# Kernel optimization log

Hardware: AMD Instinct MI355X
Metric: run time of the kernel (lower is better)

The kernel has to match this reference:

```python
import jax, jax.numpy as jnp
import numpy as np

B, T, DIM, H, KV, HD = 1, 2048, 2048, 16, 4, 128


def _rope_tables(T, hd):
    half = hd // 2
    inv_freq = 1.0 / (10000.0 ** (np.arange(0, half, dtype=np.float32) / half))
    t = np.arange(T, dtype=np.float32)
    freqs = np.outer(t, inv_freq)                # [T, hd/2]
    emb = np.concatenate([freqs, freqs], axis=-1)  # [T, hd]
    return jnp.asarray(np.cos(emb)), jnp.asarray(np.sin(emb))


def setup_inputs() -> dict:
    key = jax.random.key(0)
    kx, kq, kk, kv, ko = jax.random.split(key, 5)
    s = 0.02
    x = jax.random.normal(kx, (B, T, DIM), dtype=jnp.float32)
    wq = jax.random.normal(kq, (H * HD, DIM), dtype=jnp.float32) * s
    wk = jax.random.normal(kk, (KV * HD, DIM), dtype=jnp.float32) * s
    wv = jax.random.normal(kv, (KV * HD, DIM), dtype=jnp.float32) * s
    wo = jax.random.normal(ko, (DIM, H * HD), dtype=jnp.float32) * s
    cos, sin = _rope_tables(T, HD)
    return {"x": x, "wq": wq, "wk": wk, "wv": wv, "wo": wo, "cos": cos, "sin": sin}


def _rotate_half(u):
    u1, u2 = jnp.split(u, 2, axis=-1)
    return jnp.concatenate([-u2, u1], axis=-1)


def _apply_rope(u, cos, sin):
    # u: [B, T, h, hd]; cos/sin: [T, hd]
    c = cos[None, :, None, :]
    s = sin[None, :, None, :]
    return u * c + _rotate_half(u) * s


def reference(x, wq, wk, wv, wo, cos, sin):
    b, t, dim = x.shape
    hd = cos.shape[1]
    h = wq.shape[0] // hd
    kvh = wk.shape[0] // hd
    rep = h // kvh
    scale = hd ** -0.5

    q = (x @ wq.T).reshape(b, t, h, hd)
    k = (x @ wk.T).reshape(b, t, kvh, hd)
    v = (x @ wv.T).reshape(b, t, kvh, hd)

    q = _apply_rope(q, cos, sin)
    k = _apply_rope(k, cos, sin)

    # Group queries by shared KV head instead of materializing repeat_kv
    qg = q.reshape(b, t, kvh, rep, hd)
    scores = jnp.einsum('bqgrd,bkgd->bgrqk', qg, k) * scale  # [b,g,r,T,T]
    causal = jnp.tril(jnp.ones((t, t), dtype=bool))
    scores = jnp.where(causal[None, None, None], scores, jnp.float32(-1e30))
    attn = jax.nn.softmax(scores, axis=-1)
    out = jnp.einsum('bgrqk,bkgd->bqgrd', attn, v).reshape(b, t, h * hd)
    return out @ wo.T
```

## Files before the change

### kernel.cpp

```cpp
#include <hip/hip_runtime.h>
#include <hip/hip_bf16.h>

typedef unsigned short u16;
typedef __attribute__((ext_vector_type(8))) short bf16x8;
typedef __attribute__((ext_vector_type(8))) unsigned short u16x8;
typedef __attribute__((ext_vector_type(4))) float f32x4;

#define T_SEQ 2048
#define DIM   2048
#define NH    16
#define NKV   4
#define HD    128
#define NQKV  3072
#define SCALE 0.08838834764831845f
#define CHUNK 512

__device__ __forceinline__ u16 f2bf(float f) {
  unsigned int u = __float_as_uint(f);
  unsigned int r = (u + 0x7fffu + ((u >> 16) & 1u)) >> 16;
  return (u16)r;
}
__device__ __forceinline__ float bf2f(u16 v) {
  return __uint_as_float(((unsigned int)v) << 16);
}

#define B1 1048576
#define B2 2097152
#define B3 2359296
#define B4 2621440
#define B5 3670016
__global__ void cast_all(const float4* __restrict__ x,  const float4* __restrict__ wq,
                         const float4* __restrict__ wk, const float4* __restrict__ wv,
                         const float4* __restrict__ wo,
                         ushort4* __restrict__ xb, ushort4* __restrict__ wqkvb,
                         ushort4* __restrict__ wob) {
  int i = blockIdx.x * 256 + threadIdx.x;
  const float4* src; ushort4* dst; int j;
  if (i < B1)      { src = x;  dst = xb;               j = i; }
  else if (i < B2) { src = wq; dst = wqkvb;            j = i - B1; }
  else if (i < B3) { src = wk; dst = wqkvb + 1048576;  j = i - B2; }
  else if (i < B4) { src = wv; dst = wqkvb + 1310720;  j = i - B3; }
  else             { src = wo; dst = wob;              j = i - B4; }
  float4 v = src[j];
  ushort4 o;
  o.x = f2bf(v.x); o.y = f2bf(v.y); o.z = f2bf(v.z); o.w = f2bf(v.w);
  dst[j] = o;
}

#define BM 128
#define BN 64
#define BK 64
#define LDP 72

__global__ __launch_bounds__(256) void gemm_bt(
    const u16* __restrict__ A, const u16* __restrict__ W,
    float* __restrict__ Cf, u16* __restrict__ Cb, int M, int N, int K)
{
  __shared__ u16 As[BM * LDP];
  __shared__ u16 Bs[BN * LDP];
  const int tid  = threadIdx.x;
  const int lane = tid & 63;
  const int wave = tid >> 6;
  const int ln   = lane & 15;
  const int quad = lane >> 4;
  const int m0 = blockIdx.y * BM;
  const int n0 = blockIdx.x * BN;
  const int wm = wave * 32;

  const int sr = tid >> 3;
  const int sc = (tid & 7) * 8;

  f32x4 acc[2][4] = {};

  for (int k0 = 0; k0 < K; k0 += BK) {
#pragma unroll
    for (int c = 0; c < 4; ++c) {
      int row = c * 32 + sr;
      *(bf16x8*)&As[row * LDP + sc] =
          *(const bf16x8*)&A[(size_t)(m0 + row) * K + k0 + sc];
    }
#pragma unroll
    for (int c = 0; c < 2; ++c) {
      int row = c * 32 + sr;
      *(bf16x8*)&Bs[row * LDP + sc] =
          *(const bf16x8*)&W[(size_t)(n0 + row) * K + k0 + sc];
    }
    __syncthreads();
#pragma unroll
    for (int ks = 0; ks < 2; ++ks) {
      bf16x8 af[2], bfr[4];
#pragma unroll
      for (int mt = 0; mt < 2; ++mt)
        af[mt] = *(const bf16x8*)&As[(wm + mt * 16 + ln) * LDP + ks * 32 + quad * 8];
#pragma unroll
      for (int nt = 0; nt < 4; ++nt)
        bfr[nt] = *(const bf16x8*)&Bs[(nt * 16 + ln) * LDP + ks * 32 + quad * 8];
#pragma unroll
      for (int mt = 0; mt < 2; ++mt)
#pragma unroll
        for (int nt = 0; nt < 4; ++nt)
          acc[mt][nt] = __builtin_amdgcn_mfma_f32_16x16x32_bf16(
              af[mt], bfr[nt], acc[mt][nt], 0, 0, 0);
    }
    __syncthreads();
  }

#pragma unroll
  for (int mt = 0; mt < 2; ++mt)
#pragma unroll
    for (int nt = 0; nt < 4; ++nt)
#pragma unroll
      for (int r = 0; r < 4; ++r) {
        int row = m0 + wm + mt * 16 + quad * 4 + r;
        int col = n0 + nt * 16 + ln;
        if (Cb) Cb[(size_t)row * N + col] = f2bf(acc[mt][nt][r]);
        else    Cf[(size_t)row * N + col] = acc[mt][nt][r];
      }
}

__global__ __launch_bounds__(256) void rope_fused(
    const u16* __restrict__ QKVb, const float* __restrict__ cosT,
    const float* __restrict__ sinT, u16* __restrict__ Qs,
    u16* __restrict__ Kb, u16* __restrict__ Vt)
{
  const int blk = blockIdx.x, tid = threadIdx.x;
  if (blk < 2048) {
    int e = blk * 2048 + tid * 8;
    int t = e >> 11, rem = e & 2047;
    int h = rem >> 7, d0 = rem & 127;
    const u16* row = QKVb + (size_t)t * NQKV + h * HD;
    u16x8 v = *(const u16x8*)&row[d0];
    u16x8 p = *(const u16x8*)&row[d0 ^ 64];
    float4 c0 = *(const float4*)&cosT[t * HD + d0];
    float4 c1 = *(const float4*)&cosT[t * HD + d0 + 4];
    float4 s0 = *(const float4*)&sinT[t * HD + d0];
    float4 s1 = *(const float4*)&sinT[t * HD + d0 + 4];
    float cc[8] = {c0.x, c0.y, c0.z, c0.w, c1.x, c1.y, c1.z, c1.w};
    float ss[8] = {s0.x, s0.y, s0.z, s0.w, s1.x, s1.y, s1.z, s1.w};
    float sgn = (d0 < 64) ? -1.f : 1.f;
    u16x8 o;
#pragma unroll
    for (int j = 0; j < 8; ++j)
      o[j] = f2bf((bf2f(v[j]) * cc[j] + sgn * bf2f(p[j]) * ss[j]) * SCALE);
    *(u16x8*)&Qs[(size_t)(t * NH + h) * HD + d0] = o;
  } else if (blk < 2560) {
    int e = (blk - 2048) * 2048 + tid * 8;
    int t = e >> 9, rem = e & 511;
    int g = rem >> 7, d0 = rem & 127;
    const u16* row = QKVb + (size_t)t * NQKV + DIM + g * HD;
    u16x8 v = *(const u16x8*)&row[d0];
    u16x8 p = *(const u16x8*)&row[d0 ^ 64];
    float4 c0 = *(const float4*)&cosT[t * HD + d0];
    float4 c1 = *(const float4*)&cosT[t * HD + d0 + 4];
    float4 s0 = *(const float4*)&sinT[t * HD + d0];
    float4 s1 = *(const float4*)&sinT[t * HD + d0 + 4];
    float cc[8] = {c0.x, c0.y, c0.z, c0.w, c1.x, c1.y, c1.z, c1.w};
    float ss[8] = {s0.x, s0.y, s0.z, s0.w, s1.x, s1.y, s1.z, s1.w};
    float sgn = (d0 < 64) ? -1.f : 1.f;
    u16x8 o;
#pragma unroll
    for (int j = 0; j < 8; ++j)
      o[j] = f2bf(bf2f(v[j]) * cc[j] + sgn * bf2f(p[j]) * ss[j]);
    *(u16x8*)&Kb[((size_t)g * T_SEQ + t) * HD + d0] = o;
  } else {
    __shared__ u16 Vls[64][72];
    int bv = blk - 2560;
    int g  = bv >> 6, rem = bv & 63;
    int dt = rem >> 5, tt = rem & 31;
    int t0 = tt * 64, db = dt * 64;
    {
      int lr = tid >> 2, lc = (tid & 3) * 16;
      const u16* src = QKVb + (size_t)(t0 + lr) * NQKV + DIM + NKV * HD + g * HD + db + lc;
      *(u16x8*)&Vls[lr][lc]     = *(const u16x8*)&src[0];
      *(u16x8*)&Vls[lr][lc + 8] = *(const u16x8*)&src[8];
    }
    __syncthreads();
    {
      int dr = tid >> 2, tc = (tid & 3) * 16;
      u16x8 a, b;
#pragma unroll
      for (int j = 0; j < 8; ++j) {
        a[j] = Vls[tc + j][dr];
        b[j] = Vls[tc + 8 + j][dr];
      }
      u16* dst = Vt + (size_t)(g * HD + db + dr) * T_SEQ + t0 + tc;
      *(u16x8*)&dst[0] = a;
      *(u16x8*)&dst[8] = b;
    }
  }
}

#define KSP 136
#define VSP 72
#define PSP 72
__global__ __launch_bounds__(256) void flash_partial(
    const u16* __restrict__ Qs, const u16* __restrict__ Kb,
    const u16* __restrict__ Vt, u16* __restrict__ Opart,
    float* __restrict__ lpart)
{
  const int c  = blockIdx.x;
  const int qi = blockIdx.y;
  const int h  = blockIdx.z;
  const int b  = qi >> 2;
  if (c > b) return;
  const int g  = h >> 2;
  const int q0 = qi << 7;
  const int k0 = c << 9;
  const int kend = min(k0 + CHUNK, q0 + 128);

  __shared__ u16 Ks[64 * KSP];
  __shared__ u16 Vs[HD * VSP];
  __shared__ u16 Ps[4][32 * PSP];

  const int tid  = threadIdx.x;
  const int lane = tid & 63;
  const int w    = tid >> 6;
  const int ln   = lane & 15;
  const int quad = lane >> 4;

  bf16x8 aq[2][4];
#pragma unroll
  for (int mt = 0; mt < 2; ++mt) {
    const u16* qp = Qs + ((size_t)(q0 + w * 32 + mt * 16 + ln) * NH + h) * HD + quad * 8;
#pragma unroll
    for (int ks = 0; ks < 4; ++ks) aq[mt][ks] = *(const bf16x8*)&qp[ks * 32];
  }

  f32x4 o[2][8] = {};
  float rs[2][4] = {};

  const int rb0 = q0 + w * 32 + quad * 4;
  const int rb1 = rb0 + 16;
  const int rmax0 = q0 + w * 32 + 15;
  const int rmax1 = q0 + w * 32 + 31;

  const u16* kbase = Kb + (size_t)g * T_SEQ * HD;

  for (int jb = k0; jb < kend; jb += 64) {
    {
      int r = tid >> 4, cc = (tid & 15) * 8;
#pragma unroll
      for (int i = 0; i < 4; ++i) {
        int row = i * 16 + r;
        *(bf16x8*)&Ks[row * KSP + cc] =
            *(const bf16x8*)&kbase[(size_t)(jb + row) * HD + cc];
      }
    }
    {
      int r = tid >> 3, cc = (tid & 7) * 8;
#pragma unroll
      for (int i = 0; i < 4; ++i) {
        int row = i * 32 + r;
        *(bf16x8*)&Vs[row * VSP + cc] =
            *(const bf16x8*)&Vt[(size_t)(g * HD + row) * T_SEQ + jb + cc];
      }
    }
    __syncthreads();

    if (jb <= rmax1) {
      const bool do0  = (jb <= rmax0);
      const bool diag = (jb >= q0);

#pragma unroll
      for (int nb = 0; nb < 4; ++nb) {
        bf16x8 kf[4];
#pragma unroll
        for (int ks = 0; ks < 4; ++ks)
          kf[ks] = *(const bf16x8*)&Ks[(nb * 16 + ln) * KSP + ks * 32 + quad * 8];
        f32x4 s0 = {}, s1 = {};
#pragma unroll
        for (int ks = 0; ks < 4; ++ks) {
          if (do0) s0 = __builtin_amdgcn_mfma_f32_16x16x32_bf16(aq[0][ks], kf[ks], s0, 0, 0, 0);
          s1 = __builtin_amdgcn_mfma_f32_16x16x32_bf16(aq[1][ks], kf[ks], s1, 0, 0, 0);
        }
        const int j = jb + nb * 16 + ln;
#pragma unroll
        for (int r = 0; r < 4; ++r) {
          if (do0) {
            float p = (!diag || j <= rb0 + r) ? __expf(s0[r]) : 0.f;
            rs[0][r] += p;
            Ps[w][(quad * 4 + r) * PSP + nb * 16 + ln] = f2bf(p);
          }
          float p1 = (!diag || j <= rb1 + r) ? __expf(s1[r]) : 0.f;
          rs[1][r] += p1;
          Ps[w][(16 + quad * 4 + r) * PSP + nb * 16 + ln] = f2bf(p1);
        }
      }

#pragma unroll
      for (int kst = 0; kst < 2; ++kst) {
        bf16x8 ap0, ap1;
        if (do0) ap0 = *(const bf16x8*)&Ps[w][ln * PSP + kst * 32 + quad * 8];
        ap1 = *(const bf16x8*)&Ps[w][(16 + ln) * PSP + kst * 32 + quad * 8];
#pragma unroll
        for (int nb8 = 0; nb8 < 8; ++nb8) {
          bf16x8 bv = *(const bf16x8*)&Vs[(nb8 * 16 + ln) * VSP + kst * 32 + quad * 8];
          if (do0) o[0][nb8] = __builtin_amdgcn_mfma_f32_16x16x32_bf16(ap0, bv, o[0][nb8], 0, 0, 0);
          o[1][nb8] = __builtin_amdgcn_mfma_f32_16x16x32_bf16(ap1, bv, o[1][nb8], 0, 0, 0);
        }
      }
    }
    __syncthreads();
  }

  const int slot = h * 40 + 2 * b * (b + 1) + (qi & 3) * (b + 1) + c;
  u16*   op = Opart + (size_t)slot * (128 * 128);
  float* lp = lpart + (size_t)slot * 128;
#pragma unroll
  for (int mt = 0; mt < 2; ++mt) {
#pragma unroll
    for (int r = 0; r < 4; ++r)
#pragma unroll
      for (int off = 1; off < 16; off <<= 1)
        rs[mt][r] += __shfl_xor(rs[mt][r], off);
    int rowb = w * 32 + mt * 16 + quad * 4;
#pragma unroll
    for (int r = 0; r < 4; ++r) {
#pragma unroll
      for (int nb8 = 0; nb8 < 8; ++nb8)
        op[(rowb + r) * 128 + nb8 * 16 + ln] = f2bf(o[mt][nb8][r]);
      if (ln == 0) lp[rowb + r] = rs[mt][r];
    }
  }
}

__global__ __launch_bounds__(256) void flash_reduce(
    const u16* __restrict__ Opart, const float* __restrict__ lpart,
    u16* __restrict__ AO)
{
  const int h = blockIdx.y;
  const int tid = threadIdx.x;
  const int dgrp = tid & 15, trow = tid >> 4;
  const int t = blockIdx.x * 16 + trow;
  const int d0 = dgrp * 8;
  const int qi = t >> 7, r = t & 127;
  const int b = qi >> 2;
  const int base = h * 40 + 2 * b * (b + 1) + (qi & 3) * (b + 1);
  float so[8] = {};
  float sl = 0.f;
  for (int cc = 0; cc <= b; ++cc) {
    u16x8 ov = *(const u16x8*)&Opart[(size_t)(base + cc) * (128 * 128) + r * 128 + d0];
#pragma unroll
    for (int j = 0; j < 8; ++j) so[j] += bf2f(ov[j]);
    sl += lpart[(size_t)(base + cc) * 128 + r];
  }
  const float inv = 1.f / sl;
  u16x8 o;
#pragma unroll
  for (int j = 0; j < 8; ++j) o[j] = f2bf(so[j] * inv);
  *(u16x8*)&AO[(size_t)t * DIM + h * HD + d0] = o;
}

extern "C" void kernel_launch(void* const* d_in, const int* in_sizes, int n_in,
                              void* d_out, int out_size, void* d_ws, size_t ws_size,
                              hipStream_t stream) {
  const float* x    = (const float*)d_in[0];
  const float* wq   = (const float*)d_in[1];
  const float* wk   = (const float*)d_in[2];
  const float* wv   = (const float*)d_in[3];
  const float* wo   = (const float*)d_in[4];
  const float* cosT = (const float*)d_in[5];
  const float* sinT = (const float*)d_in[6];
  float* out = (float*)d_out;

  char* ws = (char*)d_ws;
  const size_t MB = 1024 * 1024;
  u16*   xb    = (u16*)(ws + 0 * MB);
  u16*   wqkvb = (u16*)(ws + 8 * MB);
  u16*   wob   = (u16*)(ws + 20 * MB);
  u16*   QKVb  = (u16*)(ws + 28 * MB);
  u16*   Qs    = (u16*)(ws + 8 * MB);
  u16*   Kb    = (u16*)(ws + 16 * MB);
  u16*   Vt    = (u16*)(ws + 18 * MB);
  u16*   AO    = (u16*)(ws + 0 * MB);
  u16*   Opart = (u16*)(ws + 28 * MB);
  float* lpart = (float*)(ws + 48 * MB);

  cast_all<<<B5 / 256, 256, 0, stream>>>(
      (const float4*)x, (const float4*)wq, (const float4*)wk, (const float4*)wv,
      (const float4*)wo, (ushort4*)xb, (ushort4*)wqkvb, (ushort4*)wob);

  gemm_bt<<<dim3(NQKV / BN, T_SEQ / BM), 256, 0, stream>>>(
      xb, wqkvb, nullptr, QKVb, T_SEQ, NQKV, DIM);

  rope_fused<<<2816, 256, 0, stream>>>(QKVb, cosT, sinT, Qs, Kb, Vt);

  flash_partial<<<dim3(4, 16, 16), 256, 0, stream>>>(Qs, Kb, Vt, Opart, lpart);
  flash_reduce<<<dim3(T_SEQ / 16, NH), 256, 0, stream>>>(Opart, lpart, AO);

  gemm_bt<<<dim3(DIM / BN, T_SEQ / BM), 256, 0, stream>>>(
      AO, wob, out, nullptr, T_SEQ, DIM, DIM);
}
```

Baseline: 257.6 us.

## Split-K the QKV projection GEMM and fold the partial sum into RoPE

The QKV GEMM is now split into two K halves on a third grid dimension, doubling the block count so more compute units are busy. Each half writes its own bf16 partial buffer, and the rope/transpose kernel reads both partials and adds them before applying rotary embedding or the V transpose. This adds extra global traffic for the second partial buffer and an extra bf16 rounding of each partial, which slightly changes numerics.

```diff
diff --git a/kernel.cpp b/kernel.cpp
--- a/kernel.cpp
+++ b/kernel.cpp
@@ -118,19 +118,89 @@
       }
 }
 
+__global__ __launch_bounds__(256) void gemm_qkv_sk(
+    const u16* __restrict__ A, const u16* __restrict__ W,
+    u16* __restrict__ Cp, int M, int N, int K)
+{
+  __shared__ u16 As[BM * LDP];
+  __shared__ u16 Bs[BN * LDP];
+  const int tid  = threadIdx.x;
+  const int lane = tid & 63;
+  const int wave = tid >> 6;
+  const int ln   = lane & 15;
+  const int quad = lane >> 4;
+  const int m0 = blockIdx.y * BM;
+  const int n0 = blockIdx.x * BN;
+  const int wm = wave * 32;
+  const int kBeg = blockIdx.z * (K >> 1);
+  const int kEnd = kBeg + (K >> 1);
+  u16* C = Cp + (size_t)blockIdx.z * M * N;
+
+  const int sr = tid >> 3;
+  const int sc = (tid & 7) * 8;
+
+  f32x4 acc[2][4] = {};
+
+  for (int k0 = kBeg; k0 < kEnd; k0 += BK) {
+#pragma unroll
+    for (int c = 0; c < 4; ++c) {
+      int row = c * 32 + sr;
+      *(bf16x8*)&As[row * LDP + sc] =
+          *(const bf16x8*)&A[(size_t)(m0 + row) * K + k0 + sc];
+    }
+#pragma unroll
+    for (int c = 0; c < 2; ++c) {
+      int row = c * 32 + sr;
+      *(bf16x8*)&Bs[row * LDP + sc] =
+          *(const bf16x8*)&W[(size_t)(n0 + row) * K + k0 + sc];
+    }
+    __syncthreads();
+#pragma unroll
+    for (int ks = 0; ks < 2; ++ks) {
+      bf16x8 af[2], bfr[4];
+#pragma unroll
+      for (int mt = 0; mt < 2; ++mt)
+        af[mt] = *(const bf16x8*)&As[(wm + mt * 16 + ln) * LDP + ks * 32 + quad * 8];
+#pragma unroll
+      for (int nt = 0; nt < 4; ++nt)
+        bfr[nt] = *(const bf16x8*)&Bs[(nt * 16 + ln) * LDP + ks * 32 + quad * 8];
+#pragma unroll
+      for (int mt = 0; mt < 2; ++mt)
+#pragma unroll
+        for (int nt = 0; nt < 4; ++nt)
+          acc[mt][nt] = __builtin_amdgcn_mfma_f32_16x16x32_bf16(
+              af[mt], bfr[nt], acc[mt][nt], 0, 0, 0);
+    }
+    __syncthreads();
+  }
+
+#pragma unroll
+  for (int mt = 0; mt < 2; ++mt)
+#pragma unroll
+    for (int nt = 0; nt < 4; ++nt)
+#pragma unroll
+      for (int r = 0; r < 4; ++r) {
+        int row = m0 + wm + mt * 16 + quad * 4 + r;
+        int col = n0 + nt * 16 + ln;
+        C[(size_t)row * N + col] = f2bf(acc[mt][nt][r]);
+      }
+}
+
 __global__ __launch_bounds__(256) void rope_fused(
-    const u16* __restrict__ QKVb, const float* __restrict__ cosT,
-    const float* __restrict__ sinT, u16* __restrict__ Qs,
-    u16* __restrict__ Kb, u16* __restrict__ Vt)
+    const u16* __restrict__ P0, const u16* __restrict__ P1,
+    const float* __restrict__ cosT, const float* __restrict__ sinT,
+    u16* __restrict__ Qs, u16* __restrict__ Kb, u16* __restrict__ Vt)
 {
   const int blk = blockIdx.x, tid = threadIdx.x;
   if (blk < 2048) {
     int e = blk * 2048 + tid * 8;
     int t = e >> 11, rem = e & 2047;
     int h = rem >> 7, d0 = rem & 127;
-    const u16* row = QKVb + (size_t)t * NQKV + h * HD;
-    u16x8 v = *(const u16x8*)&row[d0];
-    u16x8 p = *(const u16x8*)&row[d0 ^ 64];
+    size_t off = (size_t)t * NQKV + h * HD;
+    u16x8 va = *(const u16x8*)&P0[off + d0];
+    u16x8 vb = *(const u16x8*)&P1[off + d0];
+    u16x8 pa = *(const u16x8*)&P0[off + (d0 ^ 64)];
+    u16x8 pb = *(const u16x8*)&P1[off + (d0 ^ 64)];
     float4 c0 = *(const float4*)&cosT[t * HD + d0];
     float4 c1 = *(const float4*)&cosT[t * HD + d0 + 4];
     float4 s0 = *(const float4*)&sinT[t * HD + d0];
@@ -140,16 +210,21 @@
     float sgn = (d0 < 64) ? -1.f : 1.f;
     u16x8 o;
 #pragma unroll
-    for (int j = 0; j < 8; ++j)
-      o[j] = f2bf((bf2f(v[j]) * cc[j] + sgn * bf2f(p[j]) * ss[j]) * SCALE);
+    for (int j = 0; j < 8; ++j) {
+      float u = bf2f(va[j]) + bf2f(vb[j]);
+      float pr = bf2f(pa[j]) + bf2f(pb[j]);
+      o[j] = f2bf((u * cc[j] + sgn * pr * ss[j]) * SCALE);
+    }
     *(u16x8*)&Qs[(size_t)(t * NH + h) * HD + d0] = o;
   } else if (blk < 2560) {
     int e = (blk - 2048) * 2048 + tid * 8;
     int t = e >> 9, rem = e & 511;
     int g = rem >> 7, d0 = rem & 127;
-    const u16* row = QKVb + (size_t)t * NQKV + DIM + g * HD;
-    u16x8 v = *(const u16x8*)&row[d0];
-    u16x8 p = *(const u16x8*)&row[d0 ^ 64];
+    size_t off = (size_t)t * NQKV + DIM + g * HD;
+    u16x8 va = *(const u16x8*)&P0[off + d0];
+    u16x8 vb = *(const u16x8*)&P1[off + d0];
+    u16x8 pa = *(const u16x8*)&P0[off + (d0 ^ 64)];
+    u16x8 pb = *(const u16x8*)&P1[off + (d0 ^ 64)];
     float4 c0 = *(const float4*)&cosT[t * HD + d0];
     float4 c1 = *(const float4*)&cosT[t * HD + d0 + 4];
     float4 s0 = *(const float4*)&sinT[t * HD + d0];
@@ -159,8 +234,11 @@
     float sgn = (d0 < 64) ? -1.f : 1.f;
     u16x8 o;
 #pragma unroll
-    for (int j = 0; j < 8; ++j)
-      o[j] = f2bf(bf2f(v[j]) * cc[j] + sgn * bf2f(p[j]) * ss[j]);
+    for (int j = 0; j < 8; ++j) {
+      float u = bf2f(va[j]) + bf2f(vb[j]);
+      float pr = bf2f(pa[j]) + bf2f(pb[j]);
+      o[j] = f2bf(u * cc[j] + sgn * pr * ss[j]);
+    }
     *(u16x8*)&Kb[((size_t)g * T_SEQ + t) * HD + d0] = o;
   } else {
     __shared__ u16 Vls[64][72];
@@ -170,9 +248,17 @@
     int t0 = tt * 64, db = dt * 64;
     {
       int lr = tid >> 2, lc = (tid & 3) * 16;
-      const u16* src = QKVb + (size_t)(t0 + lr) * NQKV + DIM + NKV * HD + g * HD + db + lc;
-      *(u16x8*)&Vls[lr][lc]     = *(const u16x8*)&src[0];
-      *(u16x8*)&Vls[lr][lc + 8] = *(const u16x8*)&src[8];
+      size_t off = (size_t)(t0 + lr) * NQKV + DIM + NKV * HD + g * HD + db + lc;
+      u16x8 a0 = *(const u16x8*)&P0[off],     b0 = *(const u16x8*)&P1[off];
+      u16x8 a1 = *(const u16x8*)&P0[off + 8], b1 = *(const u16x8*)&P1[off + 8];
+      u16x8 w0, w1;
+#pragma unroll
+      for (int j = 0; j < 8; ++j) {
+        w0[j] = f2bf(bf2f(a0[j]) + bf2f(b0[j]));
+        w1[j] = f2bf(bf2f(a1[j]) + bf2f(b1[j]));
+      }
+      *(u16x8*)&Vls[lr][lc]     = w0;
+      *(u16x8*)&Vls[lr][lc + 8] = w1;
     }
     __syncthreads();
     {
@@ -368,7 +454,8 @@
   u16*   xb    = (u16*)(ws + 0 * MB);
   u16*   wqkvb = (u16*)(ws + 8 * MB);
   u16*   wob   = (u16*)(ws + 20 * MB);
-  u16*   QKVb  = (u16*)(ws + 28 * MB);
+  u16*   P0    = (u16*)(ws + 28 * MB);
+  u16*   P1    = (u16*)(ws + 40 * MB);
   u16*   Qs    = (u16*)(ws + 8 * MB);
   u16*   Kb    = (u16*)(ws + 16 * MB);
   u16*   Vt    = (u16*)(ws + 18 * MB);
@@ -380,10 +467,10 @@
       (const float4*)x, (const float4*)wq, (const float4*)wk, (const float4*)wv,
       (const float4*)wo, (ushort4*)xb, (ushort4*)wqkvb, (ushort4*)wob);
 
-  gemm_bt<<<dim3(NQKV / BN, T_SEQ / BM), 256, 0, stream>>>(
-      xb, wqkvb, nullptr, QKVb, T_SEQ, NQKV, DIM);
-
-  rope_fused<<<2816, 256, 0, stream>>>(QKVb, cosT, sinT, Qs, Kb, Vt);
+  gemm_qkv_sk<<<dim3(NQKV / BN, T_SEQ / BM, 2), 256, 0, stream>>>(
+      xb, wqkvb, P0, T_SEQ, NQKV, DIM);
+
+  rope_fused<<<2816, 256, 0, stream>>>(P0, P1, cosT, sinT, Qs, Kb, Vt);
 
   flash_partial<<<dim3(4, 16, 16), 256, 0, stream>>>(Qs, Kb, Vt, Opart, lpart);
   flash_reduce<<<dim3(T_SEQ / 16, NH), 256, 0, stream>>>(Opart, lpart, AO);
```

Result: no change. 257.3 us (-0.1%).
